# Optimization experiments

Hardware: AMD Instinct MI355X
Metric: run time of the kernel (lower is better)

## Reference

```python
import jax, jax.numpy as jnp
import numpy as np

B, D, H, K = 4096, 768, 16384, 32


def setup_inputs() -> dict:
    key = jax.random.key(0)
    k1, k2, k3 = jax.random.split(key, 3)
    return {
        "x": jax.random.normal(k1, (B, D), dtype=jnp.float32),
        "W_enc": jax.random.normal(k2, (H, D), dtype=jnp.float32) * 0.02,
        "b_enc": jnp.zeros((H,), dtype=jnp.float32),
        "W_dec": jax.random.normal(k3, (D, H), dtype=jnp.float32) * 0.02,
        "b_dec": jnp.zeros((D,), dtype=jnp.float32),
        "k": K,
    }


def reference(x, W_enc, b_enc, W_dec, b_dec, k):
    # Encode: z = ReLU(x W_enc^T + b_enc)   -> [B, H]
    z = jax.nn.relu(jnp.einsum("bd,hd->bh", x, W_enc) + b_enc)
    # Top-k mask along hidden dim (k < H)
    _, topk_idx = jax.lax.top_k(z, k)                      # [B, k]
    rows = jnp.arange(z.shape[0])[:, None]                 # [B, 1]
    mask = jnp.zeros_like(z).at[rows, topk_idx].set(1.0)   # scatter ones
    z = z * mask
    # Decode: x_hat = z W_dec^T + b_dec     -> [B, D]
    x_hat = jnp.einsum("bh,dh->bd", z, W_dec) + b_dec
    return (x_hat, z)
```

## Files before the change

kernel.cpp:

```cpp
#include <hip/hip_runtime.h>

constexpr int NB = 4096;
constexpr int ND = 768;
constexpr int NH = 16384;
constexpr int NK = 32;
constexpr int CAND_MAX = 512;
#define DELTA 0.04f

typedef __bf16 bf16x8 __attribute__((ext_vector_type(8)));
typedef float  f32x4  __attribute__((ext_vector_type(4)));

constexpr size_t OFF_XBF   = 0;
constexpr size_t OFF_WENCB = OFF_XBF   + (size_t)NB * ND * 2;
constexpr size_t OFF_WDECT = OFF_WENCB + (size_t)NH * ND * 2;
constexpr size_t OFF_CIDX  = OFF_WDECT + (size_t)NH * ND * 4;
constexpr size_t OFF_CCNT  = OFF_CIDX  + (size_t)NB * CAND_MAX * 4;
constexpr size_t OFF_ZA    = OFF_CCNT  + (size_t)NB * 4;
constexpr size_t ZA_BYTES  = (size_t)NB * NH * 2;

__device__ inline unsigned short f2bf(float f) {
  unsigned u = __float_as_uint(f);
  unsigned r = u + 0x7fffu + ((u >> 16) & 1u);
  return (unsigned short)(r >> 16);
}

__device__ __forceinline__ void gld_lds16(const unsigned short* g, unsigned short* s) {
  __builtin_amdgcn_global_load_lds((const __attribute__((address_space(1))) void*)g,
                                   (__attribute__((address_space(3))) void*)s, 16, 0, 0);
}

__global__ __launch_bounds__(256) void prep_kernel(
    const float* __restrict__ x, unsigned short* __restrict__ x_bf,
    const float* __restrict__ W_enc, unsigned short* __restrict__ wenc_bf,
    const float* __restrict__ W_dec, float* __restrict__ wdecT) {
  int b = blockIdx.x, tid = threadIdx.x;
  if (b < 1024) {
    int n4 = NB * ND / 4, stride = 1024 * 256;
    for (int i = b * 256 + tid; i < n4; i += stride) {
      float4 v = ((const float4*)x)[i];
      unsigned long long p = (unsigned long long)f2bf(v.x)
                           | ((unsigned long long)f2bf(v.y) << 16)
                           | ((unsigned long long)f2bf(v.z) << 32)
                           | ((unsigned long long)f2bf(v.w) << 48);
      ((unsigned long long*)x_bf)[i] = p;
    }
  } else if (b < 3072) {
    int n4 = NH * ND / 4, stride = 2048 * 256;
    for (int i = (b - 1024) * 256 + tid; i < n4; i += stride) {
      float4 v = ((const float4*)W_enc)[i];
      unsigned long long p = (unsigned long long)f2bf(v.x)
                           | ((unsigned long long)f2bf(v.y) << 16)
                           | ((unsigned long long)f2bf(v.z) << 32)
                           | ((unsigned long long)f2bf(v.w) << 48);
      ((unsigned long long*)wenc_bf)[i] = p;
    }
  } else {
    __shared__ float tile[32][33];
    int tb = b - 3072;
    int hb = (tb & 511) * 32, db = (tb >> 9) * 32;
    int tx = tid & 31, ty = tid >> 5;
#pragma unroll
    for (int i = 0; i < 4; ++i)
      tile[ty + i * 8][tx] = W_dec[(size_t)(db + ty + i * 8) * NH + hb + tx];
    __syncthreads();
#pragma unroll
    for (int i = 0; i < 4; ++i)
      wdecT[(size_t)(hb + ty + i * 8) * ND + db + tx] = tile[tx][ty + i * 8];
  }
}

__global__ __launch_bounds__(512) void encode_gemm_kernel(
    const unsigned short* __restrict__ Abf,
    const unsigned short* __restrict__ Bbf,
    const float* __restrict__ b_enc,
    unsigned short* __restrict__ za,
    float* __restrict__ zzero) {
  __shared__ __align__(16) unsigned short lds_all[3 * 16384];

  int bid = blockIdx.x;
  int xx = bid & 7;
  int jj = bid >> 3;
  int st = jj >> 4;
  int w  = jj & 15;
  int g  = st * 8 + xx;
  int bm = (g & 3) * 4 + (w & 3);
  int bn = (g >> 2) * 4 + (w >> 2);
  int m0 = bm * 256, n0 = bn * 256;

  int tid = threadIdx.x;
  int wid = tid >> 6, l = tid & 63;
  int wr = wid >> 2, wc = wid & 3;
  int lr = l & 15, lk = l >> 4;

#define STAGE_A(nbuf, ktile, t) do {                                              \
    int c_ = (t) * 512 + tid; int r_ = c_ >> 2;                                   \
    int lu_ = (c_ & 3) ^ ((r_ >> 1) & 3);                                         \
    gld_lds16(Abf + (size_t)(m0 + r_) * ND + (ktile) * 32 + lu_ * 8,              \
              lds_all + (nbuf) * 16384 + ((t) * 512 + (wid << 6)) * 8);           \
  } while (0)
#define STAGE_B(nbuf, ktile, t) do {                                              \
    int c_ = (t) * 512 + tid; int r_ = c_ >> 2;                                   \
    int lu_ = (c_ & 3) ^ ((r_ >> 1) & 3);                                         \
    gld_lds16(Bbf + (size_t)(n0 + r_) * ND + (ktile) * 32 + lu_ * 8,              \
              lds_all + (nbuf) * 16384 + 8192 + ((t) * 512 + (wid << 6)) * 8);    \
  } while (0)

  f32x4 acc[8][4] = {};

  STAGE_A(0, 0, 0); STAGE_A(0, 0, 1); STAGE_B(0, 0, 0); STAGE_B(0, 0, 1);
  STAGE_A(1, 1, 0); STAGE_A(1, 1, 1); STAGE_B(1, 1, 0); STAGE_B(1, 1, 1);
  asm volatile("s_waitcnt vmcnt(4)" ::: "memory");
  __builtin_amdgcn_s_barrier();
  __builtin_amdgcn_sched_barrier(0);

  int cur = 0;
  for (int kt = 0; kt < 24; ++kt) {
    int nx = cur + 2; if (nx >= 3) nx -= 3;
    const unsigned short* Ab = lds_all + cur * 16384;
    const unsigned short* Bb = Ab + 8192;
    bf16x8 aF[4], bF[4];

#pragma unroll
    for (int fj = 0; fj < 4; ++fj) {
      int row = wc * 64 + fj * 16 + lr;
      int pu = lk ^ ((row >> 1) & 3);
      bF[fj] = *(const bf16x8*)(Bb + row * 32 + pu * 8);
    }
#pragma unroll
    for (int fi = 0; fi < 4; ++fi) {
      int row = wr * 128 + fi * 16 + lr;
      int pu = lk ^ ((row >> 1) & 3);
      aF[fi] = *(const bf16x8*)(Ab + row * 32 + pu * 8);
    }
    if (kt < 22) { STAGE_A(nx, kt + 2, 0); STAGE_A(nx, kt + 2, 1); }
    if (zzero && kt < 16) {
      f32x4 zz = {0.f, 0.f, 0.f, 0.f};
#pragma unroll
      for (int z2 = 0; z2 < 2; ++z2) {
        int idx = (kt * 2 + z2) * 512 + tid;
        int row = idx >> 6, col = idx & 63;
        __builtin_nontemporal_store(zz, (f32x4*)(zzero + (size_t)(m0 + row) * NH + n0) + col);
      }
    }
    __builtin_amdgcn_s_setprio(1);
#pragma unroll
    for (int fi = 0; fi < 4; ++fi)
#pragma unroll
      for (int fj = 0; fj < 4; ++fj)
        acc[fi][fj] = __builtin_amdgcn_mfma_f32_16x16x32_bf16(aF[fi], bF[fj], acc[fi][fj], 0, 0, 0);
    __builtin_amdgcn_s_setprio(0);

#pragma unroll
    for (int fi = 0; fi < 4; ++fi) {
      int row = wr * 128 + (4 + fi) * 16 + lr;
      int pu = lk ^ ((row >> 1) & 3);
      aF[fi] = *(const bf16x8*)(Ab + row * 32 + pu * 8);
    }
    if (kt < 22) { STAGE_B(nx, kt + 2, 0); STAGE_B(nx, kt + 2, 1); }
    __builtin_amdgcn_s_setprio(1);
#pragma unroll
    for (int fi = 0; fi < 4; ++fi)
#pragma unroll
      for (int fj = 0; fj < 4; ++fj)
        acc[4 + fi][fj] = __builtin_amdgcn_mfma_f32_16x16x32_bf16(aF[fi], bF[fj], acc[4 + fi][fj], 0, 0, 0);
    __builtin_amdgcn_s_setprio(0);

    if (kt < 23) {
      if (kt == 22) asm volatile("s_waitcnt vmcnt(0)" ::: "memory");
      else          asm volatile("s_waitcnt vmcnt(4)" ::: "memory");
      __builtin_amdgcn_s_barrier();
      __builtin_amdgcn_sched_barrier(0);
    }
    cur = (cur == 2) ? 0 : cur + 1;
  }
#undef STAGE_A
#undef STAGE_B

  __syncthreads();
  unsigned short* ep = lds_all + wid * 4096;
#pragma unroll
  for (int half = 0; half < 2; ++half) {
#pragma unroll
    for (int fj = 0; fj < 4; ++fj) {
      float bias = b_enc[n0 + wc * 64 + fj * 16 + lr];
#pragma unroll
      for (int i2 = 0; i2 < 4; ++i2) {
#pragma unroll
        for (int q = 0; q < 4; ++q) {
          int row = i2 * 16 + lk * 4 + q;
          int col = fj * 16 + lr;
          float v = fmaxf(acc[half * 4 + i2][fj][q] + bias, 0.0f);
          ep[row * 64 + (((col >> 3) ^ (row & 7)) * 8) + (col & 7)] = f2bf(v);
        }
      }
    }
    __syncthreads();
#pragma unroll
    for (int t = 0; t < 8; ++t) {
      int row = t * 8 + (l >> 3);
      int u = (l & 7) ^ (row & 7);
      int4 d = *(const int4*)&ep[row * 64 + u * 8];
      *(int4*)(za + (size_t)(m0 + wr * 128 + half * 64 + row) * NH
                    + n0 + wc * 64 + (l & 7) * 8) = d;
    }
    __syncthreads();
  }
}


__device__ __forceinline__ float bisect_thr(const uint4* v, int* wcnt, int tid) {
  unsigned lo = 0u, hi = 0x7F80u;
  for (int it = 0; it < 15; ++it) {
    unsigned mid = (lo + hi) >> 1;
    int c = 0;
#pragma unroll
    for (int i = 0; i < 8; ++i) {
      const unsigned* p = (const unsigned*)&v[i];
#pragma unroll
      for (int e = 0; e < 4; ++e) {
        unsigned u = p[e];
        c += ((u & 0xFFFFu) >= mid) ? 1 : 0;
        c += ((u >> 16) >= mid) ? 1 : 0;
      }
    }
#pragma unroll
    for (int off = 32; off; off >>= 1) c += __shfl_xor(c, off, 64);
    if ((tid & 63) == 0) wcnt[tid >> 6] = c;
    __syncthreads();
    int tot = wcnt[0] + wcnt[1] + wcnt[2] + wcnt[3];
    __syncthreads();
    if (tot >= NK) {
      lo = mid;
      if (tot <= 48) break;
    } else {
      hi = mid;
    }
  }
  float thr = __uint_as_float(lo << 16) - DELTA;
  return (thr < 1e-12f) ? 1e-12f : thr;
}

__device__ __forceinline__ void topk_wave0(const float* cv, const int* ci, int cnt,
                                           float* sv, int* si, int l) {
  float lv[8]; int lh[8];
#pragma unroll
  for (int ii = 0; ii < 8; ++ii) {
    int c = l + 64 * ii;
    if (c < cnt) { lv[ii] = cv[c]; lh[ii] = ci[c]; }
    else         { lv[ii] = -1.f;  lh[ii] = 0x7fffffff; }
  }
  for (int r = 0; r < NK; ++r) {
    float bv = -1.f; int bh = 0x7fffffff; int bl = l; int bii = 0;
#pragma unroll
    for (int ii = 0; ii < 8; ++ii)
      if (lv[ii] > bv || (lv[ii] == bv && lh[ii] < bh)) { bv = lv[ii]; bh = lh[ii]; bii = ii; }
#pragma unroll
    for (int off = 32; off; off >>= 1) {
      float ov = __shfl_xor(bv, off, 64);
      int   oh = __shfl_xor(bh, off, 64);
      int   ol = __shfl_xor(bl, off, 64);
      int   oi = __shfl_xor(bii, off, 64);
      if (ov > bv || (ov == bv && oh < bh)) { bv = ov; bh = oh; bl = ol; bii = oi; }
    }
    if (l == 0) {
      if (bv > -0.5f) { sv[r] = bv; si[r] = bh; }
      else            { sv[r] = 0.f; si[r] = -1; }
    }
#pragma unroll
    for (int ii = 0; ii < 8; ++ii)
      if (ii == bii && l == bl && bv > -0.5f) lv[ii] = -1.f;
  }
}

__global__ __launch_bounds__(256) void select_kernel(const unsigned short* __restrict__ za,
                                                     int* __restrict__ cand_idx,
                                                     int* __restrict__ cand_cnt) {
  int b = blockIdx.x, tid = threadIdx.x;
  const uint4* zrow = (const uint4*)(za + (size_t)b * NH);
  uint4 v[8];
#pragma unroll
  for (int i = 0; i < 8; ++i) v[i] = zrow[tid + 256 * i];

  __shared__ int wcnt[4];
  __shared__ int lcnt;
  float thr = bisect_thr(v, wcnt, tid);
  if (tid == 0) lcnt = 0;
  __syncthreads();
#pragma unroll
  for (int i = 0; i < 8; ++i) {
    const unsigned* p = (const unsigned*)&v[i];
#pragma unroll
    for (int e = 0; e < 4; ++e) {
      unsigned u = p[e];
      int hbase = (tid + 256 * i) * 8 + e * 2;
      float f0 = __uint_as_float((u & 0xFFFFu) << 16);
      float f1 = __uint_as_float(u & 0xFFFF0000u);
      if (f0 >= thr) { int s = atomicAdd(&lcnt, 1); if (s < CAND_MAX) cand_idx[(size_t)b * CAND_MAX + s] = hbase; }
      if (f1 >= thr) { int s = atomicAdd(&lcnt, 1); if (s < CAND_MAX) cand_idx[(size_t)b * CAND_MAX + s] = hbase + 1; }
    }
  }
  __syncthreads();
  if (tid == 0) cand_cnt[b] = (lcnt < CAND_MAX) ? lcnt : CAND_MAX;
}

__device__ __forceinline__ void finalize_core(
    int b, int tid, int wid, int l, int cnt,
    const float* __restrict__ W_enc, const float* __restrict__ b_enc,
    const float* __restrict__ WdecT, const float* __restrict__ b_dec,
    const float* xr, float* cv, const int* ci, float* sv, int* si,
    float* __restrict__ zout, float* __restrict__ xhat, bool zero_z) {
  const float4* xr4 = (const float4*)xr;
  for (int c = wid; c < cnt; c += 4) {
    int h = ci[c];
    const float4* wrow4 = (const float4*)(W_enc + (size_t)h * ND);
    float4 s4 = make_float4(0.f, 0.f, 0.f, 0.f);
#pragma unroll
    for (int i = 0; i < 3; ++i) {
      float4 wv = wrow4[l + 64 * i];
      float4 xv = xr4[l + 64 * i];
      s4.x = fmaf(wv.x, xv.x, s4.x);
      s4.y = fmaf(wv.y, xv.y, s4.y);
      s4.z = fmaf(wv.z, xv.z, s4.z);
      s4.w = fmaf(wv.w, xv.w, s4.w);
    }
    float s = (s4.x + s4.y) + (s4.z + s4.w);
#pragma unroll
    for (int off = 32; off; off >>= 1) s += __shfl_xor(s, off, 64);
    if (l == 0) cv[c] = fmaxf(s + b_enc[h], 0.f);
  }
  __syncthreads();

  if (wid == 0) {
    topk_wave0(cv, ci, cnt, sv, si, l);
  } else if (zero_z) {
    float4 z4 = make_float4(0.f, 0.f, 0.f, 0.f);
    float4* zr = (float4*)(zout + (size_t)b * NH);
    for (int i = tid - 64; i < NH / 4; i += 192) zr[i] = z4;
  }
  __syncthreads();

  if (tid < NK) {
    int s = si[tid];
    if (s >= 0) zout[(size_t)b * NH + s] = sv[tid];
  }

  if (tid < ND / 4) {
    float4 a = ((const float4*)b_dec)[tid];
#pragma unroll 8
    for (int j = 0; j < NK; ++j) {
      int hj = si[j]; hj = (hj < 0) ? 0 : hj;
      float vj = sv[j];
      float4 wv = ((const float4*)(WdecT + (size_t)hj * ND))[tid];
      a.x = fmaf(vj, wv.x, a.x);
      a.y = fmaf(vj, wv.y, a.y);
      a.z = fmaf(vj, wv.z, a.z);
      a.w = fmaf(vj, wv.w, a.w);
    }
    ((float4*)(xhat + (size_t)b * ND))[tid] = a;
  }
}

__global__ __launch_bounds__(256) void finalize_kernel(
    const float* __restrict__ x, const float* __restrict__ W_enc,
    const float* __restrict__ b_enc,
    const int* __restrict__ cand_idx, const int* __restrict__ cand_cnt,
    const float* __restrict__ WdecT, const float* __restrict__ b_dec,
    float* __restrict__ zout, float* __restrict__ xhat) {
  int b = blockIdx.x, tid = threadIdx.x;
  int wid = tid >> 6, l = tid & 63;
  __shared__ __align__(16) float xr[ND];
  __shared__ float cv[CAND_MAX];
  __shared__ int   ci[CAND_MAX];
  __shared__ float sv[NK];
  __shared__ int   si[NK];

  int cnt = cand_cnt[b];
  const float4* xrow = (const float4*)(x + (size_t)b * ND);
  for (int i = tid; i < ND / 4; i += 256) ((float4*)xr)[i] = xrow[i];
  for (int c = tid; c < cnt; c += 256) ci[c] = cand_idx[(size_t)b * CAND_MAX + c];
  __syncthreads();
  finalize_core(b, tid, wid, l, cnt, W_enc, b_enc, WdecT, b_dec,
                xr, cv, ci, sv, si, zout, xhat, true);
}

__global__ __launch_bounds__(256) void fused_finalize_kernel(
    const unsigned short* __restrict__ za,
    const float* __restrict__ x, const float* __restrict__ W_enc,
    const float* __restrict__ b_enc,
    const float* __restrict__ WdecT, const float* __restrict__ b_dec,
    float* __restrict__ zout, float* __restrict__ xhat) {
  int b = blockIdx.x, tid = threadIdx.x;
  int wid = tid >> 6, l = tid & 63;
  __shared__ __align__(16) float xr[ND];
  __shared__ float cv[CAND_MAX];
  __shared__ int   ci[CAND_MAX];
  __shared__ float sv[NK];
  __shared__ int   si[NK];
  __shared__ int   wcnt[4];
  __shared__ int   lcnt;

  const uint4* zrow = (const uint4*)(za + (size_t)b * NH);
  uint4 v[8];
#pragma unroll
  for (int i = 0; i < 8; ++i) v[i] = zrow[tid + 256 * i];
  const float4* xrow = (const float4*)(x + (size_t)b * ND);
  for (int i = tid; i < ND / 4; i += 256) ((float4*)xr)[i] = xrow[i];

  float thr = bisect_thr(v, wcnt, tid);
  if (tid == 0) lcnt = 0;
  __syncthreads();
#pragma unroll
  for (int i = 0; i < 8; ++i) {
    const unsigned* p = (const unsigned*)&v[i];
#pragma unroll
    for (int e = 0; e < 4; ++e) {
      unsigned u = p[e];
      int hbase = (tid + 256 * i) * 8 + e * 2;
      float f0 = __uint_as_float((u & 0xFFFFu) << 16);
      float f1 = __uint_as_float(u & 0xFFFF0000u);
      if (f0 >= thr) { int s = atomicAdd(&lcnt, 1); if (s < CAND_MAX) ci[s] = hbase; }
      if (f1 >= thr) { int s = atomicAdd(&lcnt, 1); if (s < CAND_MAX) ci[s] = hbase + 1; }
    }
  }
  __syncthreads();
  int cnt = (lcnt < CAND_MAX) ? lcnt : CAND_MAX;

  finalize_core(b, tid, wid, l, cnt, W_enc, b_enc, WdecT, b_dec,
                xr, cv, ci, sv, si, zout, xhat, false);
}

extern "C" void kernel_launch(void* const* d_in, const int* in_sizes, int n_in,
                              void* d_out, int out_size, void* d_ws, size_t ws_size,
                              hipStream_t stream) {
  const float* x     = (const float*)d_in[0];
  const float* W_enc = (const float*)d_in[1];
  const float* b_enc = (const float*)d_in[2];
  const float* W_dec = (const float*)d_in[3];
  const float* b_dec = (const float*)d_in[4];

  float* xhat = (float*)d_out;
  float* zout = (float*)d_out + (size_t)NB * ND;

  char* ws = (char*)d_ws;
  unsigned short* x_bf    = (unsigned short*)(ws + OFF_XBF);
  unsigned short* wenc_bf = (unsigned short*)(ws + OFF_WENCB);
  float*          wdecT   = (float*)(ws + OFF_WDECT);
  int*            cidx    = (int*)(ws + OFF_CIDX);
  int*            ccnt    = (int*)(ws + OFF_CCNT);

  bool fused = ws_size >= OFF_ZA + ZA_BYTES;
  unsigned short* za = fused ? (unsigned short*)(ws + OFF_ZA)
                             : (unsigned short*)zout;

  prep_kernel<<<15360, 256, 0, stream>>>(x, x_bf, W_enc, wenc_bf, W_dec, wdecT);
  encode_gemm_kernel<<<(NB / 256) * (NH / 256), 512, 0, stream>>>(
      x_bf, wenc_bf, b_enc, za, fused ? zout : nullptr);
  if (fused) {
    fused_finalize_kernel<<<NB, 256, 0, stream>>>(za, x, W_enc, b_enc, wdecT, b_dec, zout, xhat);
  } else {
    select_kernel<<<NB, 256, 0, stream>>>(za, cidx, ccnt);
    finalize_kernel<<<NB, 256, 0, stream>>>(x, W_enc, b_enc, cidx, ccnt, wdecT, b_dec, zout, xhat);
  }
}
```

Before: 385.7 us.

## Move z zero-fill into finalize kernels, unroll candidate rescoring, shrink candidate margin

Moves the 256 MB nontemporal zero-fill of the z output out of the encode GEMM main loop and into the start of the finalize kernels. There it is issued before the threshold bisection so the stores overlap with it. The exact fp32 rescoring of candidates now handles two candidates per wave iteration with x held in registers, giving more memory-level parallelism. DELTA is lowered from 0.04 to 0.025, which may shrink the candidate set but risks missing true top-k entries when bf16 rounding error exceeds the margin.

```diff
diff --git a/kernel.cpp b/kernel.cpp
--- a/kernel.cpp
+++ b/kernel.cpp
@@ -5,7 +5,7 @@
 constexpr int NH = 16384;
 constexpr int NK = 32;
 constexpr int CAND_MAX = 512;
-#define DELTA 0.04f
+#define DELTA 0.025f
 
 typedef __bf16 bf16x8 __attribute__((ext_vector_type(8)));
 typedef float  f32x4  __attribute__((ext_vector_type(4)));
@@ -73,8 +73,7 @@
     const unsigned short* __restrict__ Abf,
     const unsigned short* __restrict__ Bbf,
     const float* __restrict__ b_enc,
-    unsigned short* __restrict__ za,
-    float* __restrict__ zzero) {
+    unsigned short* __restrict__ za) {
   __shared__ __align__(16) unsigned short lds_all[3 * 16384];
 
   int bid = blockIdx.x;
@@ -133,15 +132,6 @@
       aF[fi] = *(const bf16x8*)(Ab + row * 32 + pu * 8);
     }
     if (kt < 22) { STAGE_A(nx, kt + 2, 0); STAGE_A(nx, kt + 2, 1); }
-    if (zzero && kt < 16) {
-      f32x4 zz = {0.f, 0.f, 0.f, 0.f};
-#pragma unroll
-      for (int z2 = 0; z2 < 2; ++z2) {
-        int idx = (kt * 2 + z2) * 512 + tid;
-        int row = idx >> 6, col = idx & 63;
-        __builtin_nontemporal_store(zz, (f32x4*)(zzero + (size_t)(m0 + row) * NH + n0) + col);
-      }
-    }
     __builtin_amdgcn_s_setprio(1);
 #pragma unroll
     for (int fi = 0; fi < 4; ++fi)
@@ -207,6 +197,14 @@
   }
 }
 
+
+__device__ __forceinline__ void nt_zero_row(float* zrow, int tid) {
+  f32x4 zz = {0.f, 0.f, 0.f, 0.f};
+  f32x4* zr = (f32x4*)zrow;
+#pragma unroll
+  for (int i = 0; i < NH / 4 / 256; ++i)
+    __builtin_nontemporal_store(zz, zr + tid + 256 * i);
+}
 
 __device__ __forceinline__ float bisect_thr(const uint4* v, int* wcnt, int tid) {
   unsigned lo = 0u, hi = 0x7F80u;
@@ -308,35 +306,45 @@
     const float* __restrict__ W_enc, const float* __restrict__ b_enc,
     const float* __restrict__ WdecT, const float* __restrict__ b_dec,
     const float* xr, float* cv, const int* ci, float* sv, int* si,
-    float* __restrict__ zout, float* __restrict__ xhat, bool zero_z) {
+    float* __restrict__ zout, float* __restrict__ xhat) {
   const float4* xr4 = (const float4*)xr;
-  for (int c = wid; c < cnt; c += 4) {
-    int h = ci[c];
-    const float4* wrow4 = (const float4*)(W_enc + (size_t)h * ND);
-    float4 s4 = make_float4(0.f, 0.f, 0.f, 0.f);
+  float4 xv[3];
+#pragma unroll
+  for (int i = 0; i < 3; ++i) xv[i] = xr4[l + 64 * i];
+
+  for (int c0 = wid; c0 < cnt; c0 += 8) {
+    int c1 = c0 + 4;
+    bool has1 = (c1 < cnt);
+    int h0 = ci[c0];
+    int h1 = has1 ? ci[c1] : h0;
+    const float4* w0 = (const float4*)(W_enc + (size_t)h0 * ND);
+    const float4* w1 = (const float4*)(W_enc + (size_t)h1 * ND);
+    float4 wv0[3], wv1[3];
+#pragma unroll
+    for (int i = 0; i < 3; ++i) { wv0[i] = w0[l + 64 * i]; wv1[i] = w1[l + 64 * i]; }
+    float4 a0 = {0.f, 0.f, 0.f, 0.f}, a1 = {0.f, 0.f, 0.f, 0.f};
 #pragma unroll
     for (int i = 0; i < 3; ++i) {
-      float4 wv = wrow4[l + 64 * i];
-      float4 xv = xr4[l + 64 * i];
-      s4.x = fmaf(wv.x, xv.x, s4.x);
-      s4.y = fmaf(wv.y, xv.y, s4.y);
-      s4.z = fmaf(wv.z, xv.z, s4.z);
-      s4.w = fmaf(wv.w, xv.w, s4.w);
-    }
-    float s = (s4.x + s4.y) + (s4.z + s4.w);
-#pragma unroll
-    for (int off = 32; off; off >>= 1) s += __shfl_xor(s, off, 64);
-    if (l == 0) cv[c] = fmaxf(s + b_enc[h], 0.f);
-  }
-  __syncthreads();
-
-  if (wid == 0) {
-    topk_wave0(cv, ci, cnt, sv, si, l);
-  } else if (zero_z) {
-    float4 z4 = make_float4(0.f, 0.f, 0.f, 0.f);
-    float4* zr = (float4*)(zout + (size_t)b * NH);
-    for (int i = tid - 64; i < NH / 4; i += 192) zr[i] = z4;
-  }
+      a0.x = fmaf(wv0[i].x, xv[i].x, a0.x); a1.x = fmaf(wv1[i].x, xv[i].x, a1.x);
+      a0.y = fmaf(wv0[i].y, xv[i].y, a0.y); a1.y = fmaf(wv1[i].y, xv[i].y, a1.y);
+      a0.z = fmaf(wv0[i].z, xv[i].z, a0.z); a1.z = fmaf(wv1[i].z, xv[i].z, a1.z);
+      a0.w = fmaf(wv0[i].w, xv[i].w, a0.w); a1.w = fmaf(wv1[i].w, xv[i].w, a1.w);
+    }
+    float s0 = (a0.x + a0.y) + (a0.z + a0.w);
+    float s1 = (a1.x + a1.y) + (a1.z + a1.w);
+#pragma unroll
+    for (int off = 32; off; off >>= 1) {
+      s0 += __shfl_xor(s0, off, 64);
+      s1 += __shfl_xor(s1, off, 64);
+    }
+    if (l == 0) {
+      cv[c0] = fmaxf(s0 + b_enc[h0], 0.f);
+      if (has1) cv[c1] = fmaxf(s1 + b_enc[h1], 0.f);
+    }
+  }
+  __syncthreads();
+
+  if (wid == 0) topk_wave0(cv, ci, cnt, sv, si, l);
   __syncthreads();
 
   if (tid < NK) {
@@ -378,9 +386,10 @@
   const float4* xrow = (const float4*)(x + (size_t)b * ND);
   for (int i = tid; i < ND / 4; i += 256) ((float4*)xr)[i] = xrow[i];
   for (int c = tid; c < cnt; c += 256) ci[c] = cand_idx[(size_t)b * CAND_MAX + c];
+  nt_zero_row(zout + (size_t)b * NH, tid);
   __syncthreads();
   finalize_core(b, tid, wid, l, cnt, W_enc, b_enc, WdecT, b_dec,
-                xr, cv, ci, sv, si, zout, xhat, true);
+                xr, cv, ci, sv, si, zout, xhat);
 }
 
 __global__ __launch_bounds__(256) void fused_finalize_kernel(
@@ -405,6 +414,7 @@
   for (int i = 0; i < 8; ++i) v[i] = zrow[tid + 256 * i];
   const float4* xrow = (const float4*)(x + (size_t)b * ND);
   for (int i = tid; i < ND / 4; i += 256) ((float4*)xr)[i] = xrow[i];
+  nt_zero_row(zout + (size_t)b * NH, tid);
 
   float thr = bisect_thr(v, wcnt, tid);
   if (tid == 0) lcnt = 0;
@@ -426,7 +436,7 @@
   int cnt = (lcnt < CAND_MAX) ? lcnt : CAND_MAX;
 
   finalize_core(b, tid, wid, l, cnt, W_enc, b_enc, WdecT, b_dec,
-                xr, cv, ci, sv, si, zout, xhat, false);
+                xr, cv, ci, sv, si, zout, xhat);
 }
 
 extern "C" void kernel_launch(void* const* d_in, const int* in_sizes, int n_in,
@@ -453,8 +463,7 @@
                              : (unsigned short*)zout;
 
   prep_kernel<<<15360, 256, 0, stream>>>(x, x_bf, W_enc, wenc_bf, W_dec, wdecT);
-  encode_gemm_kernel<<<(NB / 256) * (NH / 256), 512, 0, stream>>>(
-      x_bf, wenc_bf, b_enc, za, fused ? zout : nullptr);
+  encode_gemm_kernel<<<(NB / 256) * (NH / 256), 512, 0, stream>>>(x_bf, wenc_bf, b_enc, za);
   if (fused) {
     fused_finalize_kernel<<<NB, 256, 0, stream>>>(za, x, W_enc, b_enc, wdecT, b_dec, zout, xhat);
   } else {
```

New measurement: 358.7 us. 7.0% less time.
